# Kernel tuning notes

Measured on AMD Instinct MI355X. Metric: run time of the kernel, lower is better.

## Reference

```python
import jax, jax.numpy as jnp
import numpy as np
import math

EMBED_DIM = 256
N_HEAD = 8
N_LEVELS = 4
N_POINTS = 4
HEAD_DIM = EMBED_DIM // N_HEAD
TOTAL_POINTS = N_HEAD * N_LEVELS * N_POINTS
SPATIAL = np.array([[100, 100], [50, 50], [25, 25], [13, 13]], dtype=np.int32)
BS = 2
LEN_Q = int(SPATIAL.prod(1).sum())  # 13294, encoder self-attention
LEN_V = LEN_Q


def setup_inputs() -> dict:
    key = jax.random.key(0)
    ks = jax.random.split(key, 12)
    s = 1.0 / math.sqrt(EMBED_DIM)
    inp = {
        'query': jax.random.normal(ks[0], (BS, LEN_Q, EMBED_DIM), jnp.float32),
        'reference_points': jax.random.uniform(ks[1], (BS, LEN_Q, N_LEVELS, 2), jnp.float32),
        'value': jax.random.normal(ks[2], (BS, LEN_V, EMBED_DIM), jnp.float32),
        'value_spatial_shapes': jnp.asarray(SPATIAL),
        'W_value': jax.random.normal(ks[3], (EMBED_DIM, EMBED_DIM), jnp.float32) * s,
        'b_value': jnp.zeros((EMBED_DIM,), jnp.float32),
        'W_off': jax.random.normal(ks[4], (TOTAL_POINTS * 2, EMBED_DIM), jnp.float32) * 0.01,
        'b_off': jax.random.normal(ks[5], (TOTAL_POINTS * 2,), jnp.float32),
        'W_attn': jax.random.normal(ks[6], (TOTAL_POINTS, EMBED_DIM), jnp.float32) * s,
        'b_attn': jnp.zeros((TOTAL_POINTS,), jnp.float32),
        'W_out': jax.random.normal(ks[7], (EMBED_DIM, EMBED_DIM), jnp.float32) * s,
        'b_out': jnp.zeros((EMBED_DIM,), jnp.float32),
        'zeta': jnp.ones((1, 1, 1, HEAD_DIM), jnp.float32),  # search_type='embed'
    }
    return inp


def _grid_sample_bilinear(img, gx, gy):
    """img: [B,H,W,c]; gx,gy: [B,Q,P] normalized to [-1,1].
    align_corners=False, padding_mode='zeros' (matches F.grid_sample)."""
    B, H, W, c = img.shape
    x = (gx + 1.0) * (0.5 * W) - 0.5
    y = (gy + 1.0) * (0.5 * H) - 0.5
    x0 = jnp.floor(x)
    y0 = jnp.floor(y)
    wx = (x - x0)[..., None]
    wy = (y - y0)[..., None]
    flat = img.reshape(B, H * W, c)

    def gather(xi, yi):
        m = (xi >= 0) & (xi < W) & (yi >= 0) & (yi < H)
        xi_c = jnp.clip(xi, 0, W - 1).astype(jnp.int32)
        yi_c = jnp.clip(yi, 0, H - 1).astype(jnp.int32)
        idx = (yi_c * W + xi_c).reshape(B, -1, 1)
        v = jnp.take_along_axis(flat, idx, axis=1).reshape(B, *xi.shape[1:], c)
        return v * m[..., None]

    v00 = gather(x0, y0)
    v01 = gather(x0 + 1, y0)
    v10 = gather(x0, y0 + 1)
    v11 = gather(x0 + 1, y0 + 1)
    return (v00 * (1 - wx) * (1 - wy) + v01 * wx * (1 - wy)
            + v10 * (1 - wx) * wy + v11 * wx * wy)


def reference(query, reference_points, value, value_spatial_shapes,
              W_value, b_value, W_off, b_off, W_attn, b_attn, W_out, b_out, zeta):
    bs, Len_q, _ = query.shape
    Len_v = value.shape[1]
    shapes = np.asarray(value_spatial_shapes)  # static ints

    # value projection + sparse gate (zeta, not pruned/searched)
    v = value @ W_value.T + b_value
    v = v.reshape(bs, Len_v, N_HEAD, HEAD_DIM) * zeta  # [bs,Lv,h,c]

    # sampling offsets and attention weights from query
    off = (query @ W_off.T + b_off).reshape(bs, Len_q, N_HEAD, N_LEVELS, N_POINTS, 2)
    attn = (query @ W_attn.T + b_attn).reshape(bs, Len_q, N_HEAD, N_LEVELS * N_POINTS)
    attn = jax.nn.softmax(attn, axis=-1).reshape(bs, Len_q, N_HEAD, N_LEVELS, N_POINTS)

    # reference_points last dim == 2 branch
    normalizer = jnp.asarray(shapes[:, ::-1], jnp.float32).reshape(1, 1, 1, N_LEVELS, 1, 2)  # (W,H)
    loc = reference_points.reshape(bs, Len_q, 1, N_LEVELS, 1, 2) + off / normalizer
    grids = 2.0 * loc - 1.0  # [bs,Lq,h,L,P,2]

    B = bs * N_HEAD
    out = jnp.zeros((B, Len_q, HEAD_DIM), jnp.float32)
    start = 0
    for lvl in range(N_LEVELS):
        h, w = int(shapes[lvl, 0]), int(shapes[lvl, 1])
        # [bs, h*w, nh, c] -> [bs*nh, h, w, c]
        v_l = v[:, start:start + h * w].transpose(0, 2, 1, 3).reshape(B, h, w, HEAD_DIM)
        g = grids[:, :, :, lvl].transpose(0, 2, 1, 3, 4).reshape(B, Len_q, N_POINTS, 2)
        samp = _grid_sample_bilinear(v_l, g[..., 0], g[..., 1])  # [B,Lq,P,c]
        a_l = attn[:, :, :, lvl].transpose(0, 2, 1, 3).reshape(B, Len_q, N_POINTS)
        out = out + jnp.einsum('bqpc,bqp->bqc', samp, a_l)
        start += h * w

    out = out.reshape(bs, N_HEAD, Len_q, HEAD_DIM).transpose(0, 2, 1, 3).reshape(bs, Len_q, EMBED_DIM)
    return out @ W_out.T + b_out
```

## Files before the change

### kernel.cpp

```cpp
#include <hip/hip_runtime.h>


#define LQ    13294
#define NTOK  26588
#define NE    6806528

typedef unsigned short ushort_t;
typedef __attribute__((ext_vector_type(8))) short short8;
typedef __attribute__((ext_vector_type(8))) unsigned short ushort8_t;
typedef __attribute__((ext_vector_type(4))) float float4_t;

__device__ __forceinline__ ushort_t f2b(float f) {
    unsigned int x = __float_as_uint(f);
    return (ushort_t)((x + 0x7fffu + ((x >> 16) & 1u)) >> 16);
}

__device__ __forceinline__ void gload16(const void* g, void* l) {
    __builtin_amdgcn_global_load_lds(
        (const __attribute__((address_space(1))) unsigned int*)g,
        (__attribute__((address_space(3))) unsigned int*)l, 16, 0, 0);
}

__device__ __forceinline__ void cvt_seg(const float* __restrict__ s,
                                        ushort_t* __restrict__ d,
                                        int n4, int gid, int stride) {
    const float4_t* s4 = (const float4_t*)s;
    for (int i = gid; i < n4; i += stride) {
        float4_t f = s4[i];
        ushort4 o;
        o.x = f2b(f.x); o.y = f2b(f.y); o.z = f2b(f.z); o.w = f2b(f.w);
        *(ushort4*)(d + (long)i * 4) = o;
    }
}

__global__ __launch_bounds__(256) void cvt_k(
    const float* q, const float* v, const float* Wv, const float* Wo,
    const float* Wa, const float* Wout,
    ushort_t* q_bf, ushort_t* v_bf, ushort_t* Wv_bf, ushort_t* WoWa_bf,
    ushort_t* Wout_bf)
{
    const int gid = blockIdx.x * 256 + threadIdx.x;
    const int stride = gridDim.x * 256;
    cvt_seg(q,    q_bf,            NE / 4,     gid, stride);
    cvt_seg(v,    v_bf,            NE / 4,     gid, stride);
    cvt_seg(Wv,   Wv_bf,           65536 / 4,  gid, stride);
    cvt_seg(Wo,   WoWa_bf,         65536 / 4,  gid, stride);
    cvt_seg(Wa,   WoWa_bf + 65536, 32768 / 4,  gid, stride);
    cvt_seg(Wout, Wout_bf,         65536 / 4,  gid, stride);
}

__device__ __forceinline__ void gemm_tile(
    const ushort_t* __restrict__ A,
    const ushort_t* __restrict__ W,
    int m0, int n0,
    ushort_t* As, ushort_t* Bs, float4_t acc[2][4])
{
    const int tid = threadIdx.x;
    const int w  = tid >> 6;
    const int ln = tid & 63;
    const int lr = ln >> 2;
    const int lc = (ln & 3) * 8;

    ushort_t* lA0 = As + (w * 2 + 0) * 512;
    ushort_t* lA1 = As + (w * 2 + 1) * 512;
    ushort_t* lB  = Bs + w * 512;
    const ushort_t* gA0 = A + (long)(m0 + w * 32 + lr) * 256 + lc;
    const ushort_t* gA1 = gA0 + 16 * 256;
    const ushort_t* gB  = W + (long)(n0 + w * 16 + lr) * 256 + lc;

    const int krow = (ln >> 4) * 8;
    const int fr   = ln & 15;

    for (int k0 = 0; k0 < 256; k0 += 32) {
        gload16(gA0 + k0, lA0);
        gload16(gA1 + k0, lA1);
        gload16(gB  + k0, lB);
        __syncthreads();

        short8 af[2], bfr[4];
        #pragma unroll
        for (int i = 0; i < 2; i++)
            af[i] = *(const short8*)(As + (w * 32 + i * 16 + fr) * 32 + krow);
        #pragma unroll
        for (int j = 0; j < 4; j++)
            bfr[j] = *(const short8*)(Bs + (j * 16 + fr) * 32 + krow);
        #pragma unroll
        for (int i = 0; i < 2; i++)
            #pragma unroll
            for (int j = 0; j < 4; j++)
                acc[i][j] = __builtin_amdgcn_mfma_f32_16x16x32_bf16(af[i], bfr[j], acc[i][j], 0, 0, 0);
        __syncthreads();
    }
}

__global__ __launch_bounds__(256) void gemm_fused_k(
    const ushort_t* __restrict__ q_bf, const ushort_t* __restrict__ v_bf,
    const ushort_t* __restrict__ Wv,   const ushort_t* __restrict__ WoWa,
    const float* __restrict__ b_value, const float* __restrict__ b_off,
    const float* __restrict__ b_attn,  const float* __restrict__ zeta,
    ushort_t* __restrict__ vproj, float* __restrict__ oa)
{
    __shared__ __align__(16) ushort_t As[128 * 32];
    __shared__ __align__(16) ushort_t Bs[64 * 32];

    const int z = blockIdx.z;
    const int bid = blockIdx.x;
    int x, y;
    if (z == 0) {
        if (bid >= 832) return;
        int id = (bid & 7) * 104 + (bid >> 3);
        x = id >> 2; y = id & 3;
    } else {
        int id = (bid & 7) * 156 + (bid >> 3);
        x = id / 6; y = id - x * 6;
    }
    const int m0 = x * 128;
    const int n0 = y * 64;

    float4_t acc[2][4] = {};
    gemm_tile(z ? q_bf : v_bf, z ? WoWa : Wv, m0, n0, As, Bs, acc);

    const int tid = threadIdx.x;
    const int w = tid >> 6, ln = tid & 63;
    const int col = ln & 15;
    const int rq  = (ln >> 4) * 4;
    #pragma unroll
    for (int j = 0; j < 4; j++) {
        int n = n0 + j * 16 + col;
        if (z == 0) {
            float bz = b_value[n];
            float zz = zeta[n & 31];
            long hbase = (long)(n >> 5) * NTOK;
            #pragma unroll
            for (int i = 0; i < 2; i++) {
                #pragma unroll
                for (int r = 0; r < 4; r++) {
                    int m = m0 + w * 32 + i * 16 + rq + r;
                    if (m < NTOK)
                        vproj[(hbase + m) * 32 + (n & 31)] = f2b((acc[i][j][r] + bz) * zz);
                }
            }
        } else {
            float bz = (n < 256) ? b_off[n] : b_attn[n - 256];
            #pragma unroll
            for (int i = 0; i < 2; i++) {
                #pragma unroll
                for (int r = 0; r < 4; r++) {
                    int m = m0 + w * 32 + i * 16 + rq + r;
                    if (m < NTOK) oa[(long)m * 384 + n] = acc[i][j][r] + bz;
                }
            }
        }
    }
}

__global__ __launch_bounds__(256) void gemm_out_k(
    const ushort_t* __restrict__ A,
    const ushort_t* __restrict__ W,
    const float* __restrict__ bias,
    float* __restrict__ C)
{
    __shared__ __align__(16) ushort_t As[128 * 32];
    __shared__ __align__(16) ushort_t Bs[64 * 32];

    const int bid = blockIdx.x;
    int id = (bid & 7) * 104 + (bid >> 3);
    const int m0 = (id >> 2) * 128;
    const int n0 = (id & 3) * 64;

    float4_t acc[2][4] = {};
    gemm_tile(A, W, m0, n0, As, Bs, acc);

    const int tid = threadIdx.x;
    const int w = tid >> 6, ln = tid & 63;
    const int col = ln & 15;
    const int rq  = (ln >> 4) * 4;
    #pragma unroll
    for (int j = 0; j < 4; j++) {
        int n = n0 + j * 16 + col;
        float bz = bias[n];
        #pragma unroll
        for (int i = 0; i < 2; i++) {
            #pragma unroll
            for (int r = 0; r < 4; r++) {
                int m = m0 + w * 32 + i * 16 + rq + r;
                if (m < NTOK) C[(long)m * 256 + n] = acc[i][j][r] + bz;
            }
        }
    }
}

__global__ __launch_bounds__(512) void sample_k(
    const float* __restrict__ refp,
    const ushort_t* __restrict__ v,
    const float* __restrict__ oa,
    ushort_t* __restrict__ outp)
{
    __shared__ __align__(16) int   p_ofs[576][4];
    __shared__ __align__(16) float p_w[576][4];
    const int bid = blockIdx.x;
    const int h   = bid & 7;
    const int tbase = (bid >> 3) * 32;
    const int tid = threadIdx.x;

    {
        const int tok1 = tid >> 4, p = tid & 15;
        const long t = tbase + tok1;
        if (t < NTOK) {
            const int lvl = p >> 2;
            const int Wi  = (lvl == 0) ? 100 : (lvl == 1) ? 50 : (lvl == 2) ? 25 : 13;
            const int st  = (lvl == 0) ? 0 : (lvl == 1) ? 10000 : (lvl == 2) ? 12500 : 13125;
            const float Wf = (float)Wi;
            const int b = (t >= LQ) ? 1 : 0;

            float lg = oa[t * 384 + 256 + h * 16 + p];
            float smax = lg;
            #pragma unroll
            for (int d = 1; d < 16; d <<= 1) smax = fmaxf(smax, __shfl_xor(smax, d, 64));
            float ex = __expf(lg - smax);
            float sm = ex;
            #pragma unroll
            for (int d = 1; d < 16; d <<= 1) sm += __shfl_xor(sm, d, 64);
            const float a = ex / sm;

            float ox = oa[t * 384 + h * 32 + p * 2];
            float oy = oa[t * 384 + h * 32 + p * 2 + 1];
            float rx = refp[t * 8 + lvl * 2];
            float ry = refp[t * 8 + lvl * 2 + 1];

            float x = rx * Wf + ox - 0.5f;
            float y = ry * Wf + oy - 0.5f;
            float xf = floorf(x), yf = floorf(y);
            float wx = x - xf, wy = y - yf;
            int x0 = (int)xf, y0 = (int)yf;

            float mx0 = ((unsigned)x0       < (unsigned)Wi) ? (1.f - wx) : 0.f;
            float mx1 = ((unsigned)(x0 + 1) < (unsigned)Wi) ? wx         : 0.f;
            float my0 = ((unsigned)y0       < (unsigned)Wi) ? (1.f - wy) * a : 0.f;
            float my1 = ((unsigned)(y0 + 1) < (unsigned)Wi) ? wy * a         : 0.f;
            int x0c = min(max(x0, 0), Wi - 1);
            int x1c = min(max(x0 + 1, 0), Wi - 1);
            int y0c = min(max(y0, 0), Wi - 1);
            int y1c = min(max(y0 + 1, 0), Wi - 1);

            const int hb = h * NTOK + b * LQ + st;
            const int r0 = hb + y0c * Wi, r1 = hb + y1c * Wi;
            const int su = tid + (tid >> 3);
            p_ofs[su][0] = (r0 + x0c) << 6;
            p_ofs[su][1] = (r0 + x1c) << 6;
            p_ofs[su][2] = (r1 + x0c) << 6;
            p_ofs[su][3] = (r1 + x1c) << 6;
            p_w[su][0] = mx0 * my0;
            p_w[su][1] = mx1 * my0;
            p_w[su][2] = mx0 * my1;
            p_w[su][3] = mx1 * my1;
        }
    }
    __syncthreads();

    const int tok2 = tid >> 4, l16 = tid & 15, s = l16 >> 2, g = l16 & 3;
    const long t = tbase + tok2;
    if (t < NTOK) {
        const char* vb = (const char*)v;
        const unsigned go = g * 16;
        const int ub = tok2 * 16 + s * 4;
        float4_t accA = {0.f, 0.f, 0.f, 0.f};
        float4_t accB = {0.f, 0.f, 0.f, 0.f};

        #pragma unroll
        for (int q = 0; q < 4; q++) {
            const int u = ub + q;
            const int su = u + (u >> 3);
            int4     o  = *(const int4*)p_ofs[su];
            float4_t w4 = *(const float4_t*)p_w[su];
            uint4 u00 = *(const uint4*)(vb + (unsigned)(o.x + go));
            uint4 u01 = *(const uint4*)(vb + (unsigned)(o.y + go));
            uint4 u10 = *(const uint4*)(vb + (unsigned)(o.z + go));
            uint4 u11 = *(const uint4*)(vb + (unsigned)(o.w + go));
            #define ACC8(U, WGT) \
                accA[0] += (WGT) * __uint_as_float((U).x << 16); \
                accA[1] += (WGT) * __uint_as_float((U).x & 0xffff0000u); \
                accA[2] += (WGT) * __uint_as_float((U).y << 16); \
                accA[3] += (WGT) * __uint_as_float((U).y & 0xffff0000u); \
                accB[0] += (WGT) * __uint_as_float((U).z << 16); \
                accB[1] += (WGT) * __uint_as_float((U).z & 0xffff0000u); \
                accB[2] += (WGT) * __uint_as_float((U).w << 16); \
                accB[3] += (WGT) * __uint_as_float((U).w & 0xffff0000u);
            ACC8(u00, w4.x)
            ACC8(u01, w4.y)
            ACC8(u10, w4.z)
            ACC8(u11, w4.w)
            #undef ACC8
        }

        #pragma unroll
        for (int c = 0; c < 4; c++) {
            accA[c] += __shfl_down(accA[c], 8, 64);
            accB[c] += __shfl_down(accB[c], 8, 64);
        }
        #pragma unroll
        for (int c = 0; c < 4; c++) {
            accA[c] += __shfl_down(accA[c], 4, 64);
            accB[c] += __shfl_down(accB[c], 4, 64);
        }

        if (s == 0) {
            ushort8_t o8;
            o8[0] = f2b(accA[0]); o8[1] = f2b(accA[1]);
            o8[2] = f2b(accA[2]); o8[3] = f2b(accA[3]);
            o8[4] = f2b(accB[0]); o8[5] = f2b(accB[1]);
            o8[6] = f2b(accB[2]); o8[7] = f2b(accB[3]);
            *(ushort8_t*)(outp + t * 256 + h * 32 + g * 8) = o8;
        }
    }
}

extern "C" void kernel_launch(void* const* d_in, const int* in_sizes, int n_in,
                              void* d_out, int out_size, void* d_ws, size_t ws_size,
                              hipStream_t stream)
{
    char* ws = (char*)d_ws;
    ushort_t* vproj   = (ushort_t*)ws;
    float*    oa      = (float*)(ws + (long)NE * 2);
    ushort_t* q_bf    = (ushort_t*)(ws + (long)NE * 2 + (long)NTOK * 1536);
    ushort_t* outpre  = q_bf;
    ushort_t* v_bf    = q_bf + NE;
    ushort_t* Wv_bf   = v_bf + NE;
    ushort_t* WoWa_bf = Wv_bf + 65536;
    ushort_t* Wout_bf = WoWa_bf + 98304;

    cvt_k<<<1024, 256, 0, stream>>>(
        (const float*)d_in[0], (const float*)d_in[2], (const float*)d_in[4],
        (const float*)d_in[6], (const float*)d_in[8], (const float*)d_in[10],
        q_bf, v_bf, Wv_bf, WoWa_bf, Wout_bf);

    gemm_fused_k<<<dim3(1248, 1, 2), 256, 0, stream>>>(
        q_bf, v_bf, Wv_bf, WoWa_bf,
        (const float*)d_in[5], (const float*)d_in[7], (const float*)d_in[9],
        (const float*)d_in[12], vproj, oa);

    sample_k<<<8 * 831, 512, 0, stream>>>(
        (const float*)d_in[1], vproj, oa, outpre);

    gemm_out_k<<<832, 256, 0, stream>>>(
        outpre, Wout_bf, (const float*)d_in[11], (float*)d_out);
}
```

Baseline: 222.9 us.

## Fuse fp32-to-bf16 conversion into GEMM tile loads and drop separate convert kernel

Removes the standalone conversion kernel and converts fp32 activations and weights to bf16 inside the GEMM tile loads, writing them to LDS through registers instead of async global-to-LDS loads. This avoids writing and rereading bf16 copies of query and value. The two projection GEMMs are merged into one flat grid of useful blocks with no idle z-slices. It also raises sample_k occupancy hints and reduces its unroll. The cost is that the GEMMs now read twice as many input bytes and load synchronously, losing the global_load_lds path.

```diff
diff --git a/kernel.cpp b/kernel.cpp
--- a/kernel.cpp
+++ b/kernel.cpp
@@ -15,66 +15,46 @@
     return (ushort_t)((x + 0x7fffu + ((x >> 16) & 1u)) >> 16);
 }
 
-__device__ __forceinline__ void gload16(const void* g, void* l) {
-    __builtin_amdgcn_global_load_lds(
-        (const __attribute__((address_space(1))) unsigned int*)g,
-        (__attribute__((address_space(3))) unsigned int*)l, 16, 0, 0);
-}
-
-__device__ __forceinline__ void cvt_seg(const float* __restrict__ s,
-                                        ushort_t* __restrict__ d,
-                                        int n4, int gid, int stride) {
-    const float4_t* s4 = (const float4_t*)s;
-    for (int i = gid; i < n4; i += stride) {
-        float4_t f = s4[i];
-        ushort4 o;
-        o.x = f2b(f.x); o.y = f2b(f.y); o.z = f2b(f.z); o.w = f2b(f.w);
-        *(ushort4*)(d + (long)i * 4) = o;
-    }
-}
-
-__global__ __launch_bounds__(256) void cvt_k(
-    const float* q, const float* v, const float* Wv, const float* Wo,
-    const float* Wa, const float* Wout,
-    ushort_t* q_bf, ushort_t* v_bf, ushort_t* Wv_bf, ushort_t* WoWa_bf,
-    ushort_t* Wout_bf)
-{
-    const int gid = blockIdx.x * 256 + threadIdx.x;
-    const int stride = gridDim.x * 256;
-    cvt_seg(q,    q_bf,            NE / 4,     gid, stride);
-    cvt_seg(v,    v_bf,            NE / 4,     gid, stride);
-    cvt_seg(Wv,   Wv_bf,           65536 / 4,  gid, stride);
-    cvt_seg(Wo,   WoWa_bf,         65536 / 4,  gid, stride);
-    cvt_seg(Wa,   WoWa_bf + 65536, 32768 / 4,  gid, stride);
-    cvt_seg(Wout, Wout_bf,         65536 / 4,  gid, stride);
-}
-
+__device__ __forceinline__ ushort8_t cvt8(float4_t f0, float4_t f1) {
+    ushort8_t o;
+    o[0] = f2b(f0.x); o[1] = f2b(f0.y); o[2] = f2b(f0.z); o[3] = f2b(f0.w);
+    o[4] = f2b(f1.x); o[5] = f2b(f1.y); o[6] = f2b(f1.z); o[7] = f2b(f1.w);
+    return o;
+}
+
+template<bool A_BF16>
 __device__ __forceinline__ void gemm_tile(
-    const ushort_t* __restrict__ A,
-    const ushort_t* __restrict__ W,
-    int m0, int n0,
-    ushort_t* As, ushort_t* Bs, float4_t acc[2][4])
+    const void* __restrict__ Av,
+    const float* __restrict__ Wf,
+    int m0, ushort_t* As, ushort_t* Bs, float4_t acc[2][4])
 {
     const int tid = threadIdx.x;
     const int w  = tid >> 6;
     const int ln = tid & 63;
-    const int lr = ln >> 2;
-    const int lc = (ln & 3) * 8;
-
-    ushort_t* lA0 = As + (w * 2 + 0) * 512;
-    ushort_t* lA1 = As + (w * 2 + 1) * 512;
-    ushort_t* lB  = Bs + w * 512;
-    const ushort_t* gA0 = A + (long)(m0 + w * 32 + lr) * 256 + lc;
-    const ushort_t* gA1 = gA0 + 16 * 256;
-    const ushort_t* gB  = W + (long)(n0 + w * 16 + lr) * 256 + lc;
-
+    const int sr = tid >> 2;
+    const int sc = (tid & 3) * 8;
     const int krow = (ln >> 4) * 8;
     const int fr   = ln & 15;
 
     for (int k0 = 0; k0 < 256; k0 += 32) {
-        gload16(gA0 + k0, lA0);
-        gload16(gA1 + k0, lA1);
-        gload16(gB  + k0, lB);
+        #pragma unroll
+        for (int rr = 0; rr < 128; rr += 64) {
+            const int m = m0 + sr + rr;
+            ushort8_t pk = {};
+            if (m < NTOK) {
+                if (A_BF16) {
+                    pk = *(const ushort8_t*)((const ushort_t*)Av + (long)m * 256 + k0 + sc);
+                } else {
+                    const float4_t* s4 = (const float4_t*)((const float*)Av + (long)m * 256 + k0 + sc);
+                    pk = cvt8(s4[0], s4[1]);
+                }
+            }
+            *(ushort8_t*)(As + (sr + rr) * 32 + sc) = pk;
+        }
+        {
+            const float4_t* s4 = (const float4_t*)(Wf + (long)sr * 256 + k0 + sc);
+            *(ushort8_t*)(Bs + sr * 32 + sc) = cvt8(s4[0], s4[1]);
+        }
         __syncthreads();
 
         short8 af[2], bfr[4];
@@ -94,8 +74,9 @@
 }
 
 __global__ __launch_bounds__(256) void gemm_fused_k(
-    const ushort_t* __restrict__ q_bf, const ushort_t* __restrict__ v_bf,
-    const ushort_t* __restrict__ Wv,   const ushort_t* __restrict__ WoWa,
+    const float* __restrict__ q,  const float* __restrict__ v,
+    const float* __restrict__ Wv, const float* __restrict__ Wo,
+    const float* __restrict__ Wa,
     const float* __restrict__ b_value, const float* __restrict__ b_off,
     const float* __restrict__ b_attn,  const float* __restrict__ zeta,
     ushort_t* __restrict__ vproj, float* __restrict__ oa)
@@ -103,22 +84,21 @@
     __shared__ __align__(16) ushort_t As[128 * 32];
     __shared__ __align__(16) ushort_t Bs[64 * 32];
 
-    const int z = blockIdx.z;
     const int bid = blockIdx.x;
-    int x, y;
-    if (z == 0) {
-        if (bid >= 832) return;
-        int id = (bid & 7) * 104 + (bid >> 3);
-        x = id >> 2; y = id & 3;
-    } else {
-        int id = (bid & 7) * 156 + (bid >> 3);
-        x = id / 6; y = id - x * 6;
-    }
+    const int id = (bid & 7) * 260 + (bid >> 3);
+    int z, x, y;
+    if (id < 832) { z = 0; x = id >> 2; y = id & 3; }
+    else { int id2 = id - 832; z = 1; x = id2 / 6; y = id2 - x * 6; }
     const int m0 = x * 128;
     const int n0 = y * 64;
 
+    const float* Wf;
+    if (z == 0)            Wf = Wv + (long)n0 * 256;
+    else if (n0 < 256)     Wf = Wo + (long)n0 * 256;
+    else                   Wf = Wa + (long)(n0 - 256) * 256;
+
     float4_t acc[2][4] = {};
-    gemm_tile(z ? q_bf : v_bf, z ? WoWa : Wv, m0, n0, As, Bs, acc);
+    gemm_tile<false>(z ? (const void*)q : (const void*)v, Wf, m0, As, Bs, acc);
 
     const int tid = threadIdx.x;
     const int w = tid >> 6, ln = tid & 63;
@@ -156,7 +136,7 @@
 
 __global__ __launch_bounds__(256) void gemm_out_k(
     const ushort_t* __restrict__ A,
-    const ushort_t* __restrict__ W,
+    const float* __restrict__ Wout,
     const float* __restrict__ bias,
     float* __restrict__ C)
 {
@@ -164,12 +144,12 @@
     __shared__ __align__(16) ushort_t Bs[64 * 32];
 
     const int bid = blockIdx.x;
-    int id = (bid & 7) * 104 + (bid >> 3);
+    const int id = (bid & 7) * 104 + (bid >> 3);
     const int m0 = (id >> 2) * 128;
     const int n0 = (id & 3) * 64;
 
     float4_t acc[2][4] = {};
-    gemm_tile(A, W, m0, n0, As, Bs, acc);
+    gemm_tile<true>(A, Wout + (long)n0 * 256, m0, As, Bs, acc);
 
     const int tid = threadIdx.x;
     const int w = tid >> 6, ln = tid & 63;
@@ -190,7 +170,7 @@
     }
 }
 
-__global__ __launch_bounds__(512) void sample_k(
+__global__ __launch_bounds__(512, 8) void sample_k(
     const float* __restrict__ refp,
     const ushort_t* __restrict__ v,
     const float* __restrict__ oa,
@@ -267,7 +247,7 @@
         float4_t accA = {0.f, 0.f, 0.f, 0.f};
         float4_t accB = {0.f, 0.f, 0.f, 0.f};
 
-        #pragma unroll
+        #pragma unroll 2
         for (int q = 0; q < 4; q++) {
             const int u = ub + q;
             const int su = u + (u >> 3);
@@ -322,20 +302,11 @@
     char* ws = (char*)d_ws;
     ushort_t* vproj   = (ushort_t*)ws;
     float*    oa      = (float*)(ws + (long)NE * 2);
-    ushort_t* q_bf    = (ushort_t*)(ws + (long)NE * 2 + (long)NTOK * 1536);
-    ushort_t* outpre  = q_bf;
-    ushort_t* v_bf    = q_bf + NE;
-    ushort_t* Wv_bf   = v_bf + NE;
-    ushort_t* WoWa_bf = Wv_bf + 65536;
-    ushort_t* Wout_bf = WoWa_bf + 98304;
-
-    cvt_k<<<1024, 256, 0, stream>>>(
+    ushort_t* outpre  = (ushort_t*)(ws + (long)NE * 2 + (long)NTOK * 1536);
+
+    gemm_fused_k<<<2080, 256, 0, stream>>>(
         (const float*)d_in[0], (const float*)d_in[2], (const float*)d_in[4],
-        (const float*)d_in[6], (const float*)d_in[8], (const float*)d_in[10],
-        q_bf, v_bf, Wv_bf, WoWa_bf, Wout_bf);
-
-    gemm_fused_k<<<dim3(1248, 1, 2), 256, 0, stream>>>(
-        q_bf, v_bf, Wv_bf, WoWa_bf,
+        (const float*)d_in[6], (const float*)d_in[8],
         (const float*)d_in[5], (const float*)d_in[7], (const float*)d_in[9],
         (const float*)d_in[12], vproj, oa);
 
@@ -343,5 +314,5 @@
         (const float*)d_in[1], vproj, oa, outpre);
 
     gemm_out_k<<<832, 256, 0, stream>>>(
-        outpre, Wout_bf, (const float*)d_in[11], (float*)d_out);
-}
+        outpre, (const float*)d_in[10], (const float*)d_in[11], (float*)d_out);
+}
```

Measured after the change: 218.1 us. 2.2% less time.
